# Kernel optimization log

Measured on AMD Instinct MI355X. Metric: run time of the kernel, lower is better.

## Reference

```python
import jax, jax.numpy as jnp
import numpy as np

OUT_SIZE = 7      # roi_layer out_size
SAMPLE_NUM = 2    # roi_layer sample_num (sampling grid per bin)
STRIDES = (4, 8, 16, 32)


def _roi_align_rotated(feat, rois, spatial_scale):
    """Rotated RoIAlign matching AerialDetection's CUDA kernel.
    feat: [B,C,H,W]; rois: [N,6] = (batch_idx, cx, cy, w, h, theta)."""
    B, C, H, W = feat.shape
    g, P = SAMPLE_NUM, OUT_SIZE
    dt = feat.dtype
    b = rois[:, 0].astype(jnp.int32)
    cx = rois[:, 1] * spatial_scale
    cy = rois[:, 2] * spatial_scale
    rw = rois[:, 3] * spatial_scale
    rh = rois[:, 4] * spatial_scale
    theta = rois[:, 5]
    bin_w = rw / P
    bin_h = rh / P
    pidx = jnp.arange(P, dtype=dt)
    sidx = jnp.arange(g, dtype=dt)
    # local sample offsets relative to roi center, before rotation: [N,P,g]
    off = pidx[None, :, None] + (sidx[None, None, :] + 0.5) / g
    yy = (-rh / 2)[:, None, None] + off * bin_h[:, None, None]
    xx = (-rw / 2)[:, None, None] + off * bin_w[:, None, None]
    yy = yy[:, :, None, :, None]   # [N,P,1,g,1]
    xx = xx[:, None, :, None, :]   # [N,1,P,1,g]
    ct = jnp.cos(theta)[:, None, None, None, None]
    st = jnp.sin(theta)[:, None, None, None, None]
    x = xx * ct + yy * st + cx[:, None, None, None, None]  # [N,P,P,g,g]
    y = yy * ct - xx * st + cy[:, None, None, None, None]
    valid = (y > -1.0) & (y < H) & (x > -1.0) & (x < W)
    y = jnp.maximum(y, 0.0)
    x = jnp.maximum(x, 0.0)
    y0 = jnp.minimum(jnp.floor(y).astype(jnp.int32), H - 1)
    x0 = jnp.minimum(jnp.floor(x).astype(jnp.int32), W - 1)
    y1 = jnp.minimum(y0 + 1, H - 1)
    x1 = jnp.minimum(x0 + 1, W - 1)
    y = jnp.where(y0 >= H - 1, jnp.asarray(H - 1, dt), y)
    x = jnp.where(x0 >= W - 1, jnp.asarray(W - 1, dt), x)
    ly = y - y0
    lx = x - x0
    hy = 1.0 - ly
    hx = 1.0 - lx
    flat = feat.transpose(0, 2, 3, 1).reshape(B * H * W, C)
    b5 = b[:, None, None, None, None]

    def gather(yi, xi):
        return flat[(b5 * H + yi) * W + xi]  # [N,P,P,g,g,C]

    val = (hy * hx)[..., None] * gather(y0, x0) \
        + (hy * lx)[..., None] * gather(y0, x1) \
        + (ly * hx)[..., None] * gather(y1, x0) \
        + (ly * lx)[..., None] * gather(y1, x1)
    val = jnp.where(valid[..., None], val, 0.0)
    out = val.mean(axis=(3, 4))  # average g*g samples -> [N,P,P,C]
    return out.transpose(0, 3, 1, 2)  # [N,C,P,P]


def _conv3x3(x, w, bias):
    y = jax.lax.conv_general_dilated(
        x, w, (1, 1), 'SAME', dimension_numbers=('NCHW', 'OIHW', 'NCHW'))
    return y + bias[None, :, None, None]


def setup_inputs() -> dict:
    key = jax.random.key(0)
    ks = jax.random.split(key, 12)
    B, C, N = 2, 256, 512
    img = 1024.0
    feat0 = jax.random.normal(ks[0], (B, C, 256, 256), jnp.float32)
    feat1 = jax.random.normal(ks[1], (B, C, 128, 128), jnp.float32)
    feat2 = jax.random.normal(ks[2], (B, C, 64, 64), jnp.float32)
    feat3 = jax.random.normal(ks[3], (B, C, 32, 32), jnp.float32)
    b = jax.random.randint(ks[4], (N,), 0, B).astype(jnp.float32)
    cx = jax.random.uniform(ks[5], (N,)) * img
    cy = jax.random.uniform(ks[6], (N,)) * img
    rw = 16.0 + jax.random.uniform(ks[7], (N,)) * 240.0
    rh = 16.0 + jax.random.uniform(ks[8], (N,)) * 240.0
    th = jax.random.uniform(ks[9], (N,)) * np.float32(np.pi)
    rois = jnp.stack([b, cx, cy, rw, rh, th], axis=1)
    pre_w = jax.random.normal(ks[10], (C, C, 3, 3), jnp.float32) * 0.02
    pre_b = jnp.zeros((C,), jnp.float32)
    post_w = jax.random.normal(ks[11], (C, C, 3, 3), jnp.float32) * 0.02
    post_b = jnp.zeros((C,), jnp.float32)
    return {'feat0': feat0, 'feat1': feat1, 'feat2': feat2, 'feat3': feat3,
            'rois': rois, 'pre_w': pre_w, 'pre_b': pre_b,
            'post_w': post_w, 'post_b': post_b}


def reference(feat0, feat1, feat2, feat3, rois, pre_w, pre_b, post_w, post_b):
    acc = 0.0
    for f, s in zip((feat0, feat1, feat2, feat3), STRIDES):
        t = _roi_align_rotated(f, rois, 1.0 / s)
        # pre_conv (ConvModule conv+ReLU); the module's extra ReLU is idempotent
        t = jax.nn.relu(_conv3x3(t, pre_w, pre_b))
        acc = acc + t
    # post_conv (ConvModule conv+ReLU)
    return jax.nn.relu(_conv3x3(acc, post_w, post_b))
```

## Files before the change

kernel.cpp:

```cpp
#include <hip/hip_runtime.h>
#include <hip/hip_bf16.h>

#define P 7
#define CCH 256
#define NPIX 49
#define KTOT 2304
#define TILE 25088
#define ZOFF (2 * TILE)
#define LDSZ (2 * TILE + 512)

typedef __bf16 bf16x8 __attribute__((ext_vector_type(8)));
typedef float f32x4 __attribute__((ext_vector_type(4)));

__device__ __forceinline__ unsigned short f2bf(float f) {
    unsigned int u = __float_as_uint(f);
    unsigned int r = (u + 0x7fffu + ((u >> 16) & 1u)) >> 16;
    return (unsigned short)r;
}
__device__ __forceinline__ float blo(unsigned int u) { return __uint_as_float(u << 16); }
__device__ __forceinline__ float bhi(unsigned int u) { return __uint_as_float(u & 0xffff0000u); }

__global__ void nhwc_transpose_kernel(const float* __restrict__ src,
                                      unsigned short* __restrict__ dst,
                                      int H, int W) {
    __shared__ float tile[32][33];
    int x0 = blockIdx.x * 32;
    int c0 = blockIdx.y * 32;
    int bz = blockIdx.z;
    int b = bz / H, y = bz - b * H;
    int tx = threadIdx.x & 31, ty = threadIdx.x >> 5;
    const float* s = src + ((size_t)(b * CCH + c0) * H + y) * W + x0;
#pragma unroll
    for (int j = 0; j < 4; ++j) {
        int row = ty + j * 8;
        tile[row][tx] = s[(size_t)row * H * W + tx];
    }
    __syncthreads();
    unsigned short* d = dst + ((size_t)bz * W + x0) * CCH + c0;
#pragma unroll
    for (int j = 0; j < 4; ++j) {
        int row = ty + j * 8;
        d[(size_t)row * CCH + tx] = f2bf(tile[tx][row]);
    }
}

__global__ void wtrans_kernel(const float* __restrict__ pre_w,
                              const float* __restrict__ post_w,
                              unsigned short* __restrict__ btpre,
                              unsigned short* __restrict__ btpost) {
    int idx = blockIdx.x * 256 + threadIdx.x;
    const int total = CCH * KTOT;
    if (idx >= 2 * total) return;
    const float* w = pre_w;
    unsigned short* o = btpre;
    int r = idx;
    if (r >= total) { r -= total; w = post_w; o = btpost; }
    int co = r / KTOT, k = r - co * KTOT;
    int t = k >> 8, ci = k & 255;
    o[r] = f2bf(w[(size_t)(co * CCH + ci) * 9 + t]);
}

__launch_bounds__(1024)
__global__ void fused_roi_kernel(const float* __restrict__ rois,
                                 const unsigned short* __restrict__ nh0,
                                 const unsigned short* __restrict__ nh1,
                                 const unsigned short* __restrict__ nh2,
                                 const unsigned short* __restrict__ nh3,
                                 const float* __restrict__ raw0,
                                 const float* __restrict__ raw1,
                                 const float* __restrict__ raw2,
                                 const float* __restrict__ raw3,
                                 int modes,
                                 const unsigned short* __restrict__ btpre,
                                 const unsigned short* __restrict__ btpost,
                                 const float* __restrict__ pre_b,
                                 const float* __restrict__ post_b,
                                 float* __restrict__ out) {
    __shared__ __align__(16) char lds[LDSZ];

    int roi  = blockIdx.x;
    int tid  = threadIdx.x;
    int lane = tid & 63;
    int wv   = tid >> 6;
    int lrow = lane & 15;
    int lgrp = lane >> 4;
    int ch0  = lane * 4;
    int co   = wv * 16 + lrow;

    if (tid < 128) ((float*)(lds + ZOFF))[tid] = 0.f;

    const float* rp = rois + (size_t)roi * 6;
    int   bidx = (int)rp[0];
    float cx0 = rp[1], cy0 = rp[2], rw0 = rp[3], rh0 = rp[4], th = rp[5];
    float ct = cosf(th), st = sinf(th);

    const unsigned short* nh[4] = {nh0, nh1, nh2, nh3};
    const float* raw[4] = {raw0, raw1, raw2, raw3};
    const int Hs[4] = {256, 128, 64, 32};
    const float scl[4] = {0.25f, 0.125f, 0.0625f, 0.03125f};

    auto ra_pair = [&](int p) {
        int ml = wv & 1;
        int gl = p * 2 + ml;
        int H = Hs[gl], W = H;
        float s = scl[gl];
        float cx = cx0 * s, cy = cy0 * s, rw = rw0 * s, rh = rh0 * s;
        float bw = rw * (1.0f / P), bh = rh * (1.0f / P);
        float fH = (float)H, fW = (float)W;
        bool staged = (modes >> gl) & 1;
        const unsigned short* f = nh[gl];
        const float* fr = raw[gl];
        for (int bin = (wv >> 1); bin < NPIX; bin += 8) {
            int py = bin / 7, px = bin - py * 7;
            float a0 = 0.f, a1 = 0.f, a2 = 0.f, a3 = 0.f;
#pragma unroll
            for (int smp = 0; smp < 4; ++smp) {
                int sy = smp >> 1, sx = smp & 1;
                float offy = (float)py + 0.25f + 0.5f * (float)sy;
                float offx = (float)px + 0.25f + 0.5f * (float)sx;
                float yy = offy * bh - rh * 0.5f;
                float xx = offx * bw - rw * 0.5f;
                float X = xx * ct + yy * st + cx;
                float Y = yy * ct - xx * st + cy;
                if (Y > -1.0f && Y < fH && X > -1.0f && X < fW) {
                    float Yc = fmaxf(Y, 0.f), Xc = fmaxf(X, 0.f);
                    int y0 = min((int)Yc, H - 1);
                    int x0 = min((int)Xc, W - 1);
                    int y1 = min(y0 + 1, H - 1), x1 = min(x0 + 1, W - 1);
                    if (y0 >= H - 1) Yc = (float)(H - 1);
                    if (x0 >= W - 1) Xc = (float)(W - 1);
                    float ly = Yc - (float)y0, lx = Xc - (float)x0;
                    float hy = 1.f - ly, hx = 1.f - lx;
                    float w00 = hy * hx, w01 = hy * lx, w10 = ly * hx, w11 = ly * lx;
                    if (staged) {
                        size_t r0 = (size_t)(bidx * H + y0) * W;
                        size_t r1 = (size_t)(bidx * H + y1) * W;
                        uint2 u00 = *(const uint2*)(f + ((r0 + x0) << 8) + ch0);
                        uint2 u01 = *(const uint2*)(f + ((r0 + x1) << 8) + ch0);
                        uint2 u10 = *(const uint2*)(f + ((r1 + x0) << 8) + ch0);
                        uint2 u11 = *(const uint2*)(f + ((r1 + x1) << 8) + ch0);
                        a0 += w00 * blo(u00.x) + w01 * blo(u01.x) + w10 * blo(u10.x) + w11 * blo(u11.x);
                        a1 += w00 * bhi(u00.x) + w01 * bhi(u01.x) + w10 * bhi(u10.x) + w11 * bhi(u11.x);
                        a2 += w00 * blo(u00.y) + w01 * blo(u01.y) + w10 * blo(u10.y) + w11 * blo(u11.y);
                        a3 += w00 * bhi(u00.y) + w01 * bhi(u01.y) + w10 * bhi(u10.y) + w11 * bhi(u11.y);
                    } else {
                        size_t hw = (size_t)H * W;
                        size_t i00 = (size_t)y0 * W + x0, i01 = (size_t)y0 * W + x1;
                        size_t i10 = (size_t)y1 * W + x0, i11 = (size_t)y1 * W + x1;
                        const float* fp0 = fr + ((size_t)bidx * CCH + ch0) * hw;
                        float* accp[4] = {&a0, &a1, &a2, &a3};
#pragma unroll
                        for (int cc = 0; cc < 4; ++cc) {
                            const float* fp = fp0 + (size_t)cc * hw;
                            *accp[cc] += w00 * fp[i00] + w01 * fp[i01] + w10 * fp[i10] + w11 * fp[i11];
                        }
                    }
                }
            }
            unsigned int q01 = (unsigned)f2bf(a0 * 0.25f) | ((unsigned)f2bf(a1 * 0.25f) << 16);
            unsigned int q23 = (unsigned)f2bf(a2 * 0.25f) | ((unsigned)f2bf(a3 * 0.25f) << 16);
            int off = ml * TILE + bin * 512 + ((lane * 8) ^ ((bin & 7) << 4));
            *(uint2*)(lds + off) = make_uint2(q01, q23);
        }
    };

    int pys[4], pxs[4];
    bool prow[4];
#pragma unroll
    for (int mt = 0; mt < 4; ++mt) {
        int pix = mt * 16 + lrow;
        pys[mt] = pix / 7;
        pxs[mt] = pix - pys[mt] * 7;
        prow[mt] = pix < NPIX;
    }
    int lg16 = lgrp * 16;

    auto conv_pair = [&](const unsigned short* __restrict__ Bt, f32x4 (&acc)[2][4]) {
        const f32x4 FZ = {0.f, 0.f, 0.f, 0.f};
#pragma unroll
        for (int lv = 0; lv < 2; ++lv)
#pragma unroll
            for (int mt = 0; mt < 4; ++mt) acc[lv][mt] = FZ;
        const unsigned short* bp = Bt + (size_t)co * KTOT + lgrp * 8;
        for (int t = 0; t < 9; ++t) {
            int dy = t / 3 - 1, dx = (t % 3) - 1;
            int roff[4], swz[4];
#pragma unroll
            for (int mt = 0; mt < 4; ++mt) {
                int oy = pys[mt] + dy, ox = pxs[mt] + dx;
                bool v = prow[mt] && ((unsigned)oy < 7u) && ((unsigned)ox < 7u);
                int np = oy * 7 + ox;
                roff[mt] = v ? np * 512 : (ZOFF - 0);
                swz[mt]  = v ? ((np & 7) << 4) : 16;
                if (!v) roff[mt] = ZOFF;
            }
#pragma unroll
            for (int c8 = 0; c8 < 8; ++c8) {
                int kb = c8 * 64 + lg16;
                int ke = (t * 8 + c8) * 32;
                bf16x8 b = *(const bf16x8*)(bp + ke);
#pragma unroll
                for (int mt = 0; mt < 4; ++mt) {
                    int lo = kb ^ swz[mt];
                    bf16x8 a0 = *(const bf16x8*)(lds + roff[mt] + lo);
                    acc[0][mt] = __builtin_amdgcn_mfma_f32_16x16x32_bf16(a0, b, acc[0][mt], 0, 0, 0);
                    bf16x8 a1 = *(const bf16x8*)(lds + (roff[mt] == ZOFF ? ZOFF : roff[mt] + TILE) + lo);
                    acc[1][mt] = __builtin_amdgcn_mfma_f32_16x16x32_bf16(a1, b, acc[1][mt], 0, 0, 0);
                }
            }
        }
    };

    float bs_pre = pre_b[co];
    f32x4 sum[4];
    {
        const f32x4 FZ = {0.f, 0.f, 0.f, 0.f};
#pragma unroll
        for (int mt = 0; mt < 4; ++mt) sum[mt] = FZ;
    }

    ra_pair(0);
    __syncthreads();
    {
        f32x4 acc[2][4];
        conv_pair(btpre, acc);
#pragma unroll
        for (int lv = 0; lv < 2; ++lv)
#pragma unroll
            for (int mt = 0; mt < 4; ++mt)
#pragma unroll
                for (int r = 0; r < 4; ++r)
                    sum[mt][r] += fmaxf(acc[lv][mt][r] + bs_pre, 0.f);
    }
    __syncthreads();

    ra_pair(1);
    __syncthreads();
    {
        f32x4 acc[2][4];
        conv_pair(btpre, acc);
#pragma unroll
        for (int lv = 0; lv < 2; ++lv)
#pragma unroll
            for (int mt = 0; mt < 4; ++mt)
#pragma unroll
                for (int r = 0; r < 4; ++r)
                    sum[mt][r] += fmaxf(acc[lv][mt][r] + bs_pre, 0.f);
    }
    __syncthreads();

#pragma unroll
    for (int mt = 0; mt < 4; ++mt)
#pragma unroll
        for (int r = 0; r < 4; ++r) {
            int pix = mt * 16 + lgrp * 4 + r;
            if (pix < NPIX) {
                int off = pix * 512 + ((co * 2) ^ ((pix & 7) << 4));
                *(unsigned short*)(lds + off) = f2bf(sum[mt][r]);
            }
        }
    __syncthreads();

    f32x4 pacc[4];
    {
        const f32x4 FZ = {0.f, 0.f, 0.f, 0.f};
#pragma unroll
        for (int mt = 0; mt < 4; ++mt) pacc[mt] = FZ;
    }
    {
        const unsigned short* bp = btpost + (size_t)co * KTOT + lgrp * 8;
        for (int t = 0; t < 9; ++t) {
            int dy = t / 3 - 1, dx = (t % 3) - 1;
            int roff[4], swz[4];
#pragma unroll
            for (int mt = 0; mt < 4; ++mt) {
                int oy = pys[mt] + dy, ox = pxs[mt] + dx;
                bool v = prow[mt] && ((unsigned)oy < 7u) && ((unsigned)ox < 7u);
                int np = oy * 7 + ox;
                roff[mt] = v ? np * 512 : ZOFF;
                swz[mt]  = v ? ((np & 7) << 4) : 16;
            }
#pragma unroll
            for (int c8 = 0; c8 < 8; ++c8) {
                int kb = c8 * 64 + lg16;
                int ke = (t * 8 + c8) * 32;
                bf16x8 b = *(const bf16x8*)(bp + ke);
#pragma unroll
                for (int mt = 0; mt < 4; ++mt) {
                    bf16x8 a = *(const bf16x8*)(lds + roff[mt] + (kb ^ swz[mt]));
                    pacc[mt] = __builtin_amdgcn_mfma_f32_16x16x32_bf16(a, b, pacc[mt], 0, 0, 0);
                }
            }
        }
    }

    float bs_post = post_b[co];
    float* og = out + (size_t)roi * (NPIX * CCH);
#pragma unroll
    for (int mt = 0; mt < 4; ++mt)
#pragma unroll
        for (int r = 0; r < 4; ++r) {
            int pix = mt * 16 + lgrp * 4 + r;
            if (pix < NPIX)
                og[co * NPIX + pix] = fmaxf(pacc[mt][r] + bs_post, 0.f);
        }
}

extern "C" void kernel_launch(void* const* d_in, const int* in_sizes, int n_in,
                              void* d_out, int out_size, void* d_ws, size_t ws_size,
                              hipStream_t stream) {
    const float* feats[4] = {(const float*)d_in[0], (const float*)d_in[1],
                             (const float*)d_in[2], (const float*)d_in[3]};
    const float* rois   = (const float*)d_in[4];
    const float* pre_w  = (const float*)d_in[5];
    const float* pre_b  = (const float*)d_in[6];
    const float* post_w = (const float*)d_in[7];
    const float* post_b = (const float*)d_in[8];

    int nroi = in_sizes[4] / 6;
    int B = in_sizes[0] / (CCH * 256 * 256);
    const int Hs[4] = {256, 128, 64, 32};

    char* ws = (char*)d_ws;
    size_t off = 0;
    auto take = [&](size_t bytes) -> void* {
        void* p = ws + off;
        off += (bytes + 255) & ~(size_t)255;
        return p;
    };
    unsigned short* btpre  = (unsigned short*)take((size_t)CCH * KTOT * 2);
    unsigned short* btpost = (unsigned short*)take((size_t)CCH * KTOT * 2);

    unsigned short* nh[4] = {nullptr, nullptr, nullptr, nullptr};
    int modes = 0;
    for (int l = 0; l < 4; ++l) {
        size_t need = (size_t)B * Hs[l] * Hs[l] * CCH * 2;
        if (off + need <= ws_size) {
            nh[l] = (unsigned short*)take(need);
            modes |= (1 << l);
        }
    }

    for (int l = 0; l < 4; ++l) {
        if (!(modes & (1 << l))) continue;
        dim3 g(Hs[l] / 32, CCH / 32, B * Hs[l]);
        nhwc_transpose_kernel<<<g, 256, 0, stream>>>(feats[l], nh[l], Hs[l], Hs[l]);
    }
    wtrans_kernel<<<(2 * CCH * KTOT + 255) / 256, 256, 0, stream>>>(pre_w, post_w, btpre, btpost);

    fused_roi_kernel<<<nroi, 1024, 0, stream>>>(rois, nh[0], nh[1], nh[2], nh[3],
                                                feats[0], feats[1], feats[2], feats[3],
                                                modes, btpre, btpost, pre_b, post_b,
                                                (float*)d_out);
}
```

Baseline: 387.8 us.

## Halve block to 512 threads with two output-channel tiles per wave

The fused RoI kernel now runs 8 waves instead of 16. Each wave computes two 16-channel output tiles (co and co+128), so every LDS A-fragment load feeds two MFMAs. The RoI-align bin loop stride is adjusted to match the fewer waves. This cuts LDS read traffic per MFMA, but doubles accumulator registers per thread and halves the threads doing the sampling and gather phase. The launch bound of 4 waves per SIMD may force register spilling.

```diff
diff --git a/kernel.cpp b/kernel.cpp
--- a/kernel.cpp
+++ b/kernel.cpp
@@ -5,6 +5,7 @@
 #define CCH 256
 #define NPIX 49
 #define KTOT 2304
+#define THREADS 512
 #define TILE 25088
 #define ZOFF (2 * TILE)
 #define LDSZ (2 * TILE + 512)
@@ -60,7 +61,7 @@
     o[r] = f2bf(w[(size_t)(co * CCH + ci) * 9 + t]);
 }
 
-__launch_bounds__(1024)
+__launch_bounds__(THREADS, 4)
 __global__ void fused_roi_kernel(const float* __restrict__ rois,
                                  const unsigned short* __restrict__ nh0,
                                  const unsigned short* __restrict__ nh1,
@@ -85,7 +86,8 @@
     int lrow = lane & 15;
     int lgrp = lane >> 4;
     int ch0  = lane * 4;
-    int co   = wv * 16 + lrow;
+    int co0  = wv * 16 + lrow;
+    int co1  = co0 + 128;
 
     if (tid < 128) ((float*)(lds + ZOFF))[tid] = 0.f;
 
@@ -110,7 +112,7 @@
         bool staged = (modes >> gl) & 1;
         const unsigned short* f = nh[gl];
         const float* fr = raw[gl];
-        for (int bin = (wv >> 1); bin < NPIX; bin += 8) {
+        for (int bin = (wv >> 1); bin < NPIX; bin += 4) {
             int py = bin / 7, px = bin - py * 7;
             float a0 = 0.f, a1 = 0.f, a2 = 0.f, a3 = 0.f;
 #pragma unroll
@@ -175,100 +177,16 @@
     }
     int lg16 = lgrp * 16;
 
-    auto conv_pair = [&](const unsigned short* __restrict__ Bt, f32x4 (&acc)[2][4]) {
+    auto conv_pair = [&](const unsigned short* __restrict__ Bt, f32x4 (&acc)[2][4][2]) {
         const f32x4 FZ = {0.f, 0.f, 0.f, 0.f};
 #pragma unroll
         for (int lv = 0; lv < 2; ++lv)
 #pragma unroll
-            for (int mt = 0; mt < 4; ++mt) acc[lv][mt] = FZ;
-        const unsigned short* bp = Bt + (size_t)co * KTOT + lgrp * 8;
-        for (int t = 0; t < 9; ++t) {
-            int dy = t / 3 - 1, dx = (t % 3) - 1;
-            int roff[4], swz[4];
-#pragma unroll
             for (int mt = 0; mt < 4; ++mt) {
-                int oy = pys[mt] + dy, ox = pxs[mt] + dx;
-                bool v = prow[mt] && ((unsigned)oy < 7u) && ((unsigned)ox < 7u);
-                int np = oy * 7 + ox;
-                roff[mt] = v ? np * 512 : (ZOFF - 0);
-                swz[mt]  = v ? ((np & 7) << 4) : 16;
-                if (!v) roff[mt] = ZOFF;
-            }
-#pragma unroll
-            for (int c8 = 0; c8 < 8; ++c8) {
-                int kb = c8 * 64 + lg16;
-                int ke = (t * 8 + c8) * 32;
-                bf16x8 b = *(const bf16x8*)(bp + ke);
-#pragma unroll
-                for (int mt = 0; mt < 4; ++mt) {
-                    int lo = kb ^ swz[mt];
-                    bf16x8 a0 = *(const bf16x8*)(lds + roff[mt] + lo);
-                    acc[0][mt] = __builtin_amdgcn_mfma_f32_16x16x32_bf16(a0, b, acc[0][mt], 0, 0, 0);
-                    bf16x8 a1 = *(const bf16x8*)(lds + (roff[mt] == ZOFF ? ZOFF : roff[mt] + TILE) + lo);
-                    acc[1][mt] = __builtin_amdgcn_mfma_f32_16x16x32_bf16(a1, b, acc[1][mt], 0, 0, 0);
-                }
-            }
-        }
-    };
-
-    float bs_pre = pre_b[co];
-    f32x4 sum[4];
-    {
-        const f32x4 FZ = {0.f, 0.f, 0.f, 0.f};
-#pragma unroll
-        for (int mt = 0; mt < 4; ++mt) sum[mt] = FZ;
-    }
-
-    ra_pair(0);
-    __syncthreads();
-    {
-        f32x4 acc[2][4];
-        conv_pair(btpre, acc);
-#pragma unroll
-        for (int lv = 0; lv < 2; ++lv)
-#pragma unroll
-            for (int mt = 0; mt < 4; ++mt)
-#pragma unroll
-                for (int r = 0; r < 4; ++r)
-                    sum[mt][r] += fmaxf(acc[lv][mt][r] + bs_pre, 0.f);
-    }
-    __syncthreads();
-
-    ra_pair(1);
-    __syncthreads();
-    {
-        f32x4 acc[2][4];
-        conv_pair(btpre, acc);
-#pragma unroll
-        for (int lv = 0; lv < 2; ++lv)
-#pragma unroll
-            for (int mt = 0; mt < 4; ++mt)
-#pragma unroll
-                for (int r = 0; r < 4; ++r)
-                    sum[mt][r] += fmaxf(acc[lv][mt][r] + bs_pre, 0.f);
-    }
-    __syncthreads();
-
-#pragma unroll
-    for (int mt = 0; mt < 4; ++mt)
-#pragma unroll
-        for (int r = 0; r < 4; ++r) {
-            int pix = mt * 16 + lgrp * 4 + r;
-            if (pix < NPIX) {
-                int off = pix * 512 + ((co * 2) ^ ((pix & 7) << 4));
-                *(unsigned short*)(lds + off) = f2bf(sum[mt][r]);
-            }
-        }
-    __syncthreads();
-
-    f32x4 pacc[4];
-    {
-        const f32x4 FZ = {0.f, 0.f, 0.f, 0.f};
-#pragma unroll
-        for (int mt = 0; mt < 4; ++mt) pacc[mt] = FZ;
-    }
-    {
-        const unsigned short* bp = btpost + (size_t)co * KTOT + lgrp * 8;
+                acc[lv][mt][0] = FZ; acc[lv][mt][1] = FZ;
+            }
+        const unsigned short* bp0 = Bt + (size_t)co0 * KTOT + lg16 / 2;
+        const unsigned short* bp1 = Bt + (size_t)co1 * KTOT + lg16 / 2;
         for (int t = 0; t < 9; ++t) {
             int dy = t / 3 - 1, dx = (t % 3) - 1;
             int roff[4], swz[4];
@@ -284,25 +202,127 @@
             for (int c8 = 0; c8 < 8; ++c8) {
                 int kb = c8 * 64 + lg16;
                 int ke = (t * 8 + c8) * 32;
-                bf16x8 b = *(const bf16x8*)(bp + ke);
+                bf16x8 b0 = *(const bf16x8*)(bp0 + ke);
+                bf16x8 b1 = *(const bf16x8*)(bp1 + ke);
+#pragma unroll
+                for (int mt = 0; mt < 4; ++mt) {
+                    int lo = kb ^ swz[mt];
+                    bf16x8 a0 = *(const bf16x8*)(lds + roff[mt] + lo);
+                    bf16x8 a1 = *(const bf16x8*)(lds + (roff[mt] == ZOFF ? ZOFF : roff[mt] + TILE) + lo);
+                    acc[0][mt][0] = __builtin_amdgcn_mfma_f32_16x16x32_bf16(a0, b0, acc[0][mt][0], 0, 0, 0);
+                    acc[0][mt][1] = __builtin_amdgcn_mfma_f32_16x16x32_bf16(a0, b1, acc[0][mt][1], 0, 0, 0);
+                    acc[1][mt][0] = __builtin_amdgcn_mfma_f32_16x16x32_bf16(a1, b0, acc[1][mt][0], 0, 0, 0);
+                    acc[1][mt][1] = __builtin_amdgcn_mfma_f32_16x16x32_bf16(a1, b1, acc[1][mt][1], 0, 0, 0);
+                }
+            }
+        }
+    };
+
+    float bs0 = pre_b[co0], bs1 = pre_b[co1];
+    f32x4 sum[4][2];
+    {
+        const f32x4 FZ = {0.f, 0.f, 0.f, 0.f};
+#pragma unroll
+        for (int mt = 0; mt < 4; ++mt) { sum[mt][0] = FZ; sum[mt][1] = FZ; }
+    }
+
+    ra_pair(0);
+    __syncthreads();
+    {
+        f32x4 acc[2][4][2];
+        conv_pair(btpre, acc);
+#pragma unroll
+        for (int lv = 0; lv < 2; ++lv)
+#pragma unroll
+            for (int mt = 0; mt < 4; ++mt)
+#pragma unroll
+                for (int r = 0; r < 4; ++r) {
+                    sum[mt][0][r] += fmaxf(acc[lv][mt][0][r] + bs0, 0.f);
+                    sum[mt][1][r] += fmaxf(acc[lv][mt][1][r] + bs1, 0.f);
+                }
+    }
+    __syncthreads();
+
+    ra_pair(1);
+    __syncthreads();
+    {
+        f32x4 acc[2][4][2];
+        conv_pair(btpre, acc);
+#pragma unroll
+        for (int lv = 0; lv < 2; ++lv)
+#pragma unroll
+            for (int mt = 0; mt < 4; ++mt)
+#pragma unroll
+                for (int r = 0; r < 4; ++r) {
+                    sum[mt][0][r] += fmaxf(acc[lv][mt][0][r] + bs0, 0.f);
+                    sum[mt][1][r] += fmaxf(acc[lv][mt][1][r] + bs1, 0.f);
+                }
+    }
+    __syncthreads();
+
+#pragma unroll
+    for (int nt = 0; nt < 2; ++nt) {
+        int co = nt ? co1 : co0;
+#pragma unroll
+        for (int mt = 0; mt < 4; ++mt)
+#pragma unroll
+            for (int r = 0; r < 4; ++r) {
+                int pix = mt * 16 + lgrp * 4 + r;
+                if (pix < NPIX) {
+                    int off = pix * 512 + ((co * 2) ^ ((pix & 7) << 4));
+                    *(unsigned short*)(lds + off) = f2bf(sum[mt][nt][r]);
+                }
+            }
+    }
+    __syncthreads();
+
+    f32x4 pacc[4][2];
+    {
+        const f32x4 FZ = {0.f, 0.f, 0.f, 0.f};
+#pragma unroll
+        for (int mt = 0; mt < 4; ++mt) { pacc[mt][0] = FZ; pacc[mt][1] = FZ; }
+    }
+    {
+        const unsigned short* bp0 = btpost + (size_t)co0 * KTOT + lg16 / 2;
+        const unsigned short* bp1 = btpost + (size_t)co1 * KTOT + lg16 / 2;
+        for (int t = 0; t < 9; ++t) {
+            int dy = t / 3 - 1, dx = (t % 3) - 1;
+            int roff[4], swz[4];
+#pragma unroll
+            for (int mt = 0; mt < 4; ++mt) {
+                int oy = pys[mt] + dy, ox = pxs[mt] + dx;
+                bool v = prow[mt] && ((unsigned)oy < 7u) && ((unsigned)ox < 7u);
+                int np = oy * 7 + ox;
+                roff[mt] = v ? np * 512 : ZOFF;
+                swz[mt]  = v ? ((np & 7) << 4) : 16;
+            }
+#pragma unroll
+            for (int c8 = 0; c8 < 8; ++c8) {
+                int kb = c8 * 64 + lg16;
+                int ke = (t * 8 + c8) * 32;
+                bf16x8 b0 = *(const bf16x8*)(bp0 + ke);
+                bf16x8 b1 = *(const bf16x8*)(bp1 + ke);
 #pragma unroll
                 for (int mt = 0; mt < 4; ++mt) {
                     bf16x8 a = *(const bf16x8*)(lds + roff[mt] + (kb ^ swz[mt]));
-                    pacc[mt] = __builtin_amdgcn_mfma_f32_16x16x32_bf16(a, b, pacc[mt], 0, 0, 0);
-                }
-            }
-        }
-    }
-
-    float bs_post = post_b[co];
+                    pacc[mt][0] = __builtin_amdgcn_mfma_f32_16x16x32_bf16(a, b0, pacc[mt][0], 0, 0, 0);
+                    pacc[mt][1] = __builtin_amdgcn_mfma_f32_16x16x32_bf16(a, b1, pacc[mt][1], 0, 0, 0);
+                }
+            }
+        }
+    }
+
+    float pb0 = post_b[co0], pb1 = post_b[co1];
     float* og = out + (size_t)roi * (NPIX * CCH);
 #pragma unroll
     for (int mt = 0; mt < 4; ++mt)
 #pragma unroll
         for (int r = 0; r < 4; ++r) {
             int pix = mt * 16 + lgrp * 4 + r;
-            if (pix < NPIX)
-                og[co * NPIX + pix] = fmaxf(pacc[mt][r] + bs_post, 0.f);
+            if (pix < NPIX) {
+                og[co0 * NPIX + pix] = fmaxf(pacc[mt][0][r] + pb0, 0.f);
+                og[co1 * NPIX + pix] = fmaxf(pacc[mt][1][r] + pb1, 0.f);
+            }
         }
 }
 
@@ -348,8 +368,8 @@
     }
     wtrans_kernel<<<(2 * CCH * KTOT + 255) / 256, 256, 0, stream>>>(pre_w, post_w, btpre, btpost);
 
-    fused_roi_kernel<<<nroi, 1024, 0, stream>>>(rois, nh[0], nh[1], nh[2], nh[3],
-                                                feats[0], feats[1], feats[2], feats[3],
-                                                modes, btpre, btpost, pre_b, post_b,
-                                                (float*)d_out);
-}
+    fused_roi_kernel<<<nroi, THREADS, 0, stream>>>(rois, nh[0], nh[1], nh[2], nh[3],
+                                                   feats[0], feats[1], feats[2], feats[3],
+                                                   modes, btpre, btpost, pre_b, post_b,
+                                                   (float*)d_out);
+}
```

Result: no change. 381.4 us (-1.7%).
